# Kernel tuning notes

Hardware: AMD Instinct MI355X
Metric: run time of the kernel (lower is better)

Reference implementation:

```python
import itertools
import jax, jax.numpy as jnp
import numpy as np

EPS = 1.1920928955078125e-07  # torch.finfo(float32).eps, used by torchmetrics SI-SNR


def setup_inputs() -> dict:
    key = jax.random.key(0)
    k1, k2 = jax.random.split(key)
    B, S, T = 32, 2, 256000
    preds = jax.random.normal(k1, (B, S, T), dtype=jnp.float32)
    targets = jax.random.normal(k2, (B, S, T), dtype=jnp.float32)
    return {"preds": preds, "targets": targets}


def _pit_sisnr_loss(preds, targets):
    # preds, targets: [B, S, T]
    B, S, T = preds.shape
    # torchmetrics SI-SNR zero-means both signals along time
    p = preds - jnp.mean(preds, axis=-1, keepdims=True)
    t = targets - jnp.mean(targets, axis=-1, keepdims=True)
    # pairwise statistics: pred i vs target j
    dot = jnp.einsum('bit,bjt->bij', p, t)          # <p_i, t_j>        [B,S,S]
    tt = jnp.sum(t * t, axis=-1)                    # ||t_j||^2          [B,S]
    pp = jnp.sum(p * p, axis=-1)                    # ||p_i||^2          [B,S]
    alpha = dot / (tt[:, None, :] + EPS)            # projection scale   [B,S,S]
    s_target = alpha * alpha * tt[:, None, :]       # ||alpha * t||^2
    # ||p - alpha*t||^2 expanded (no [B,S,S,T] intermediate)
    noise = pp[:, :, None] - 2.0 * alpha * dot + s_target
    sisnr = 10.0 * jnp.log10((s_target + EPS) / (noise + EPS))  # [B,S,S]
    # PIT: max over all speaker permutations of the mean matched SI-SNR
    perms = np.array(list(itertools.permutations(range(S))))    # [P,S]
    rows = np.arange(S)[None, :]                                # [1,S]
    perm_scores = sisnr[:, rows, perms].mean(axis=-1)           # [B,P]
    best = perm_scores.max(axis=-1)                             # [B]
    return -jnp.mean(best)


def reference(preds, targets):
    return _pit_sisnr_loss(preds, targets)
```

## Files before the change

kernel.cpp:

```cpp
#include <hip/hip_runtime.h>

#define EPS 1.1920928955078125e-07f

#define BB 32
#define TT 256000
#define CHUNKS 50
#define T4 (TT / 4)
#define CHUNK (T4 / CHUNKS)
#define ITERS (CHUNK / 256)
#define NBLK (BB * CHUNKS)


__global__ __launch_bounds__(256, 4) void pit_partials(
    const float* __restrict__ preds, const float* __restrict__ targets,
    float* __restrict__ ws)
{
    const int b = blockIdx.x / CHUNKS;
    const int c = blockIdx.x % CHUNKS;

    const float4* p0 = (const float4*)(preds   + (size_t)(b * 2 + 0) * TT);
    const float4* p1 = (const float4*)(preds   + (size_t)(b * 2 + 1) * TT);
    const float4* t0 = (const float4*)(targets + (size_t)(b * 2 + 0) * TT);
    const float4* t1 = (const float4*)(targets + (size_t)(b * 2 + 1) * TT);

    float acc[12];
#pragma unroll
    for (int k = 0; k < 12; ++k) acc[k] = 0.f;

    const int base = c * CHUNK + (int)threadIdx.x;
#pragma unroll
    for (int it = 0; it < ITERS; ++it) {
        const int i = base + it * 256;
        float4 a0 = p0[i];
        float4 a1 = p1[i];
        float4 b0 = t0[i];
        float4 b1 = t1[i];
#pragma unroll
        for (int e = 0; e < 4; ++e) {
            float u0 = (&a0.x)[e], u1 = (&a1.x)[e];
            float v0 = (&b0.x)[e], v1 = (&b1.x)[e];
            acc[0]  += u0;       acc[1]  += u1;
            acc[2]  += v0;       acc[3]  += v1;
            acc[4]  += u0 * u0;  acc[5]  += u1 * u1;
            acc[6]  += v0 * v0;  acc[7]  += v1 * v1;
            acc[8]  += u0 * v0;  acc[9]  += u0 * v1;
            acc[10] += u1 * v0;  acc[11] += u1 * v1;
        }
    }

    const int lane = threadIdx.x & 63;
    const int wave = threadIdx.x >> 6;
#pragma unroll
    for (int k = 0; k < 12; ++k) {
        float v = acc[k];
        for (int off = 32; off > 0; off >>= 1) v += __shfl_down(v, off);
        acc[k] = v;
    }

    __shared__ float lds[4][12];
    if (lane == 0) {
#pragma unroll
        for (int k = 0; k < 12; ++k) lds[wave][k] = acc[k];
    }
    __syncthreads();

    if (threadIdx.x < 12) {
        float v = lds[0][threadIdx.x] + lds[1][threadIdx.x]
                + lds[2][threadIdx.x] + lds[3][threadIdx.x];
        ws[(size_t)blockIdx.x * 12 + threadIdx.x] = v;
    }
}

__global__ __launch_bounds__(256) void pit_final(
    const float* __restrict__ ws, float* __restrict__ out)
{
    __shared__ float sums[BB * 12];
    __shared__ float bests[BB];

    for (int s = threadIdx.x; s < BB * 12; s += 256) {
        const int b = s / 12;
        const int k = s % 12;
        float v = 0.f;
        const float* base = ws + (size_t)(b * CHUNKS) * 12 + k;
#pragma unroll 10
        for (int c = 0; c < CHUNKS; ++c) v += base[(size_t)c * 12];
        sums[s] = v;
    }
    __syncthreads();

    if (threadIdx.x < BB) {
        const float* w = sums + threadIdx.x * 12;
        const float invT = 1.0f / (float)TT;
        float pp0 = w[4] - w[0] * w[0] * invT;
        float pp1 = w[5] - w[1] * w[1] * invT;
        float tt0 = w[6] - w[2] * w[2] * invT;
        float tt1 = w[7] - w[3] * w[3] * invT;
        float d00 = w[8]  - w[0] * w[2] * invT;
        float d01 = w[9]  - w[0] * w[3] * invT;
        float d10 = w[10] - w[1] * w[2] * invT;
        float d11 = w[11] - w[1] * w[3] * invT;

        auto sisnr = [](float dot, float pp, float tt) -> float {
            float alpha = dot / (tt + EPS);
            float st    = alpha * alpha * tt;
            float noise = pp - 2.0f * alpha * dot + st;
            return 10.0f * log10f((st + EPS) / (noise + EPS));
        };
        float s00 = sisnr(d00, pp0, tt0);
        float s01 = sisnr(d01, pp0, tt1);
        float s10 = sisnr(d10, pp1, tt0);
        float s11 = sisnr(d11, pp1, tt1);

        float perm0 = 0.5f * (s00 + s11);
        float perm1 = 0.5f * (s01 + s10);
        bests[threadIdx.x] = fmaxf(perm0, perm1);
    }
    __syncthreads();

    if (threadIdx.x == 0) {
        float acc = 0.f;
#pragma unroll
        for (int b = 0; b < BB; ++b) acc += bests[b];
        out[0] = -acc / (float)BB;
    }
}

extern "C" void kernel_launch(void* const* d_in, const int* in_sizes, int n_in,
                              void* d_out, int out_size, void* d_ws, size_t ws_size,
                              hipStream_t stream)
{
    const float* preds   = (const float*)d_in[0];
    const float* targets = (const float*)d_in[1];
    float* out = (float*)d_out;
    float* ws  = (float*)d_ws;

    pit_partials<<<dim3(NBLK), dim3(256), 0, stream>>>(preds, targets, ws);
    pit_final<<<dim3(1), dim3(256), 0, stream>>>(ws, out);
}
```

Measured before the change: 146.9 us.

## Stage inputs via direct global-to-LDS loads with smaller per-block chunks

Each wave now streams one of the four signals (two preds, two targets) straight into shared memory with global_load_lds. All of a block's loads are issued up front, and the accumulation then reads the data back from LDS. The chunk size per block becomes fixed at 512 float4, which raises the block count, and the occupancy hint is raised to 8 blocks per CU. The aim is more memory-level parallelism and more loads in flight for this bandwidth-bound reduction. In exchange it uses 32KB of LDS per block, which may limit the occupancy actually reached, and the final kernel must sum more partials per batch.

Result: no change. 145.9 us (-0.7%).

```diff
diff --git a/kernel.cpp b/kernel.cpp
--- a/kernel.cpp
+++ b/kernel.cpp
@@ -4,37 +4,61 @@
 
 #define BB 32
 #define TT 256000
-#define CHUNKS 50
 #define T4 (TT / 4)
-#define CHUNK (T4 / CHUNKS)
+#define CHUNK 512
+#define CHUNKS (T4 / CHUNK)
+#define NBLK (BB * CHUNKS)
 #define ITERS (CHUNK / 256)
-#define NBLK (BB * CHUNKS)
+#define SEGS (CHUNK / 64)
 
 
-__global__ __launch_bounds__(256, 4) void pit_partials(
+__device__ __forceinline__ void gload16(const float4* g, float4* l)
+{
+    __builtin_amdgcn_global_load_lds(
+        (const __attribute__((address_space(1))) void*)(const void*)g,
+        (__attribute__((address_space(3))) void*)(void*)l,
+        16, 0, 0);
+}
+
+__global__ __launch_bounds__(256, 8) void pit_partials(
     const float* __restrict__ preds, const float* __restrict__ targets,
     float* __restrict__ ws)
 {
+    __shared__ float4 lds4[4 * CHUNK];
+    float* f = (float*)lds4;
+
+    const int tid  = threadIdx.x;
+    const int lane = tid & 63;
+    const int wave = tid >> 6;
+
     const int b = blockIdx.x / CHUNKS;
     const int c = blockIdx.x % CHUNKS;
 
-    const float4* p0 = (const float4*)(preds   + (size_t)(b * 2 + 0) * TT);
-    const float4* p1 = (const float4*)(preds   + (size_t)(b * 2 + 1) * TT);
-    const float4* t0 = (const float4*)(targets + (size_t)(b * 2 + 0) * TT);
-    const float4* t1 = (const float4*)(targets + (size_t)(b * 2 + 1) * TT);
+    const float* sb =
+        (wave == 0) ? preds   + (size_t)(b * 2 + 0) * TT :
+        (wave == 1) ? preds   + (size_t)(b * 2 + 1) * TT :
+        (wave == 2) ? targets + (size_t)(b * 2 + 0) * TT :
+                      targets + (size_t)(b * 2 + 1) * TT;
+
+    const float4* g = (const float4*)sb + (size_t)c * CHUNK + lane;
+    float4* l = &lds4[wave * CHUNK];
+#pragma unroll
+    for (int k = 0; k < SEGS; ++k)
+        gload16(g + k * 64, l + k * 64);
+
+    __syncthreads();
 
     float acc[12];
 #pragma unroll
     for (int k = 0; k < 12; ++k) acc[k] = 0.f;
 
-    const int base = c * CHUNK + (int)threadIdx.x;
 #pragma unroll
     for (int it = 0; it < ITERS; ++it) {
-        const int i = base + it * 256;
-        float4 a0 = p0[i];
-        float4 a1 = p1[i];
-        float4 b0 = t0[i];
-        float4 b1 = t1[i];
+        const int i = it * 256 + tid;
+        float4 a0 = lds4[0 * CHUNK + i];
+        float4 a1 = lds4[1 * CHUNK + i];
+        float4 b0 = lds4[2 * CHUNK + i];
+        float4 b1 = lds4[3 * CHUNK + i];
 #pragma unroll
         for (int e = 0; e < 4; ++e) {
             float u0 = (&a0.x)[e], u1 = (&a1.x)[e];
@@ -48,8 +72,6 @@
         }
     }
 
-    const int lane = threadIdx.x & 63;
-    const int wave = threadIdx.x >> 6;
 #pragma unroll
     for (int k = 0; k < 12; ++k) {
         float v = acc[k];
@@ -57,17 +79,16 @@
         acc[k] = v;
     }
 
-    __shared__ float lds[4][12];
+    __syncthreads();
     if (lane == 0) {
 #pragma unroll
-        for (int k = 0; k < 12; ++k) lds[wave][k] = acc[k];
+        for (int k = 0; k < 12; ++k) f[wave * 12 + k] = acc[k];
     }
     __syncthreads();
 
-    if (threadIdx.x < 12) {
-        float v = lds[0][threadIdx.x] + lds[1][threadIdx.x]
-                + lds[2][threadIdx.x] + lds[3][threadIdx.x];
-        ws[(size_t)blockIdx.x * 12 + threadIdx.x] = v;
+    if (tid < 12) {
+        float v = f[0 + tid] + f[12 + tid] + f[24 + tid] + f[36 + tid];
+        ws[(size_t)blockIdx.x * 12 + tid] = v;
     }
 }
 
@@ -82,7 +103,7 @@
         const int k = s % 12;
         float v = 0.f;
         const float* base = ws + (size_t)(b * CHUNKS) * 12 + k;
-#pragma unroll 10
+#pragma unroll 25
         for (int c = 0; c < CHUNKS; ++c) v += base[(size_t)c * 12];
         sums[s] = v;
     }
```

## Stream inputs through LDS with async global_load_lds double-buffering per wave

Applied to the files above, without the earlier changes.

Each wavefront now owns its own contiguous chunk and stages the four input streams into a per-wave double-buffered LDS region using global_load_lds. Explicit vmcnt waits overlap the next tile's loads with the current tile's accumulation. The block-level LDS reduction and its barrier are removed: each wave writes its 12 partials directly, and occupancy hints rise to 8 blocks per CU. The cost is extra LDS traffic, and the direct-to-LDS path may not beat plain unrolled float4 loads on a kernel that is purely bandwidth-bound.

Measured after the change: 147.7 us. About the same (+0.5%).

```diff
diff --git a/kernel.cpp b/kernel.cpp
--- a/kernel.cpp
+++ b/kernel.cpp
@@ -4,37 +4,73 @@
 
 #define BB 32
 #define TT 256000
-#define CHUNKS 50
 #define T4 (TT / 4)
-#define CHUNK (T4 / CHUNKS)
-#define ITERS (CHUNK / 256)
-#define NBLK (BB * CHUNKS)
+#define WPB 50
+#define ITW 20
+#define WCHUNK (ITW * 64)
+#define NWAVE (BB * WPB)
+#define NBLK (NWAVE / 4)
 
 
-__global__ __launch_bounds__(256, 4) void pit_partials(
+__device__ __forceinline__ void gload16(const float4* g, float4* l)
+{
+    __builtin_amdgcn_global_load_lds(
+        (const __attribute__((address_space(1))) void*)(const void*)g,
+        (__attribute__((address_space(3))) void*)(void*)l,
+        16, 0, 0);
+}
+
+__global__ __launch_bounds__(256, 8) void pit_partials(
     const float* __restrict__ preds, const float* __restrict__ targets,
     float* __restrict__ ws)
 {
-    const int b = blockIdx.x / CHUNKS;
-    const int c = blockIdx.x % CHUNKS;
+    __shared__ float4 lds4[4 * 512];
+
+    const int tid  = threadIdx.x;
+    const int lane = tid & 63;
+    const int wave = tid >> 6;
+    const int w = blockIdx.x * 4 + wave;
+    const int b = w / WPB;
+    const int s = w % WPB;
 
     const float4* p0 = (const float4*)(preds   + (size_t)(b * 2 + 0) * TT);
     const float4* p1 = (const float4*)(preds   + (size_t)(b * 2 + 1) * TT);
     const float4* t0 = (const float4*)(targets + (size_t)(b * 2 + 0) * TT);
     const float4* t1 = (const float4*)(targets + (size_t)(b * 2 + 1) * TT);
 
+    const int base = s * WCHUNK + lane;
+    float4* ldsw = &lds4[wave * 512];
+
+#define STAGE(j) do {                                   \
+        const int _off = base + (j) * 64;               \
+        float4* _d = ldsw + (((j) & 1) * 256);          \
+        gload16(p0 + _off, _d);                         \
+        gload16(p1 + _off, _d + 64);                    \
+        gload16(t0 + _off, _d + 128);                   \
+        gload16(t1 + _off, _d + 192);                   \
+    } while (0)
+
     float acc[12];
 #pragma unroll
     for (int k = 0; k < 12; ++k) acc[k] = 0.f;
 
-    const int base = c * CHUNK + (int)threadIdx.x;
+    STAGE(0);
+
 #pragma unroll
-    for (int it = 0; it < ITERS; ++it) {
-        const int i = base + it * 256;
-        float4 a0 = p0[i];
-        float4 a1 = p1[i];
-        float4 b0 = t0[i];
-        float4 b1 = t1[i];
+    for (int it = 0; it < ITW; ++it) {
+        if (it + 1 < ITW) {
+            STAGE(it + 1);
+            asm volatile("s_waitcnt vmcnt(4)" ::: "memory");
+        } else {
+            asm volatile("s_waitcnt vmcnt(0)" ::: "memory");
+        }
+        __builtin_amdgcn_sched_barrier(0);
+
+        const int i = ((it & 1) * 256) + lane;
+        float4 a0 = ldsw[i      ];
+        float4 a1 = ldsw[i +  64];
+        float4 b0 = ldsw[i + 128];
+        float4 b1 = ldsw[i + 192];
 #pragma unroll
         for (int e = 0; e < 4; ++e) {
             float u0 = (&a0.x)[e], u1 = (&a1.x)[e];
@@ -47,9 +83,8 @@
             acc[10] += u1 * v0;  acc[11] += u1 * v1;
         }
     }
+#undef STAGE
 
-    const int lane = threadIdx.x & 63;
-    const int wave = threadIdx.x >> 6;
 #pragma unroll
     for (int k = 0; k < 12; ++k) {
         float v = acc[k];
@@ -57,17 +92,10 @@
         acc[k] = v;
     }
 
-    __shared__ float lds[4][12];
     if (lane == 0) {
+        float* o = ws + (size_t)w * 12;
 #pragma unroll
-        for (int k = 0; k < 12; ++k) lds[wave][k] = acc[k];
-    }
-    __syncthreads();
-
-    if (threadIdx.x < 12) {
-        float v = lds[0][threadIdx.x] + lds[1][threadIdx.x]
-                + lds[2][threadIdx.x] + lds[3][threadIdx.x];
-        ws[(size_t)blockIdx.x * 12 + threadIdx.x] = v;
+        for (int k = 0; k < 12; ++k) o[k] = acc[k];
     }
 }
 
@@ -81,9 +109,9 @@
         const int b = s / 12;
         const int k = s % 12;
         float v = 0.f;
-        const float* base = ws + (size_t)(b * CHUNKS) * 12 + k;
+        const float* base = ws + (size_t)(b * WPB) * 12 + k;
 #pragma unroll 10
-        for (int c = 0; c < CHUNKS; ++c) v += base[(size_t)c * 12];
+        for (int c = 0; c < WPB; ++c) v += base[(size_t)c * 12];
         sums[s] = v;
     }
     __syncthreads();
```
